# Kernel tuning notes

Measured on AMD Instinct MI355X. Metric: run time of the kernel, lower is better.

## Reference

```python
import jax, jax.numpy as jnp
import numpy as np

B, S, HID = 1, 2048, 2048
H, KV, D = 16, 8, 128          # heads, kv heads, head_dim
EPS = 1e-6
THETA_T, THETA_HW = 1000000.0, 10000.0
SCALE = D ** -0.5
NEG = -1e9


def _rms(x, w):
    xf = x.astype(jnp.float32)
    var = jnp.mean(xf * xf, axis=-1, keepdims=True)
    return (w * (xf * jax.lax.rsqrt(var + EPS))).astype(x.dtype)


def _rope_cs(pos, theta, half_dim):
    # Module builds RoPE with head_dim = 2*half_dim then takes every-other freq:
    # exponents arange(0, 2*half_dim, 4) / (2*half_dim)  -> half_dim//2 freqs
    dim2 = 2 * half_dim
    inv_freq = 1.0 / theta ** (jnp.arange(0, dim2, 4, dtype=jnp.float32) / dim2)
    freqs = pos.astype(jnp.float32)[:, None] * inv_freq[None, :]   # [S, half_dim//2]
    emb = jnp.concatenate([freqs, freqs], axis=-1)                 # [S, half_dim]
    return jnp.cos(emb), jnp.sin(emb)


def _rot_half(x):
    d = x.shape[-1] // 2
    return jnp.concatenate([-x[..., d:], x[..., :d]], axis=-1)


def _apply_rope(q, k, cos, sin):
    cos = cos[None, None]  # [1,1,S,dim]
    sin = sin[None, None]
    return q * cos + _rot_half(q) * sin, k * cos + _rot_half(k) * sin


def setup_inputs() -> dict:
    key = jax.random.key(0)
    ks = jax.random.split(key, 10)
    hidden_states = jax.random.normal(ks[0], (B, S, HID), jnp.float32)
    indexes = jax.random.randint(ks[1], (3, S), 0, S)
    causal = jnp.tril(jnp.ones((S, S), bool))
    attention_mask = jnp.where(causal, 0.0, NEG).astype(jnp.float32)[None, None]
    qkv_w = jax.random.normal(ks[2], ((H + 2 * KV) * D, HID), jnp.float32) * 0.02
    qkv_b = jax.random.normal(ks[3], ((H + 2 * KV) * D,), jnp.float32) * 0.02
    o_w = jax.random.normal(ks[4], (HID, H * D), jnp.float32) * 0.02
    o_b = jax.random.normal(ks[5], (HID,), jnp.float32) * 0.02
    q_norm_w = jnp.ones((D // 2,), jnp.float32)
    k_norm_w = jnp.ones((D // 2,), jnp.float32)
    q_norm_hw_w = jnp.ones((D // 2,), jnp.float32)
    k_norm_hw_w = jnp.ones((D // 2,), jnp.float32)
    return dict(hidden_states=hidden_states, indexes=indexes, attention_mask=attention_mask,
                qkv_w=qkv_w, qkv_b=qkv_b, o_w=o_w, o_b=o_b,
                q_norm_w=q_norm_w, k_norm_w=k_norm_w,
                q_norm_hw_w=q_norm_hw_w, k_norm_hw_w=k_norm_hw_w)


def reference(hidden_states, indexes, attention_mask, qkv_w, qkv_b, o_w, o_b,
              q_norm_w, k_norm_w, q_norm_hw_w, k_norm_hw_w):
    b, s, _ = hidden_states.shape
    qkv = hidden_states @ qkv_w.T + qkv_b
    q, k, v = jnp.split(qkv, [H * D, H * D + KV * D], axis=-1)
    q = q.reshape(b, s, H, D)
    k = k.reshape(b, s, KV, D)
    v = v.reshape(b, s, KV, D)

    # split head_dim into time half and hw half
    q_t, q_hw = jnp.split(q, 2, axis=-1)
    k_t, k_hw = jnp.split(k, 2, axis=-1)
    q_t = jnp.swapaxes(_rms(q_t, q_norm_w), 1, 2)       # [B,H,S,D/2]
    k_t = jnp.swapaxes(_rms(k_t, k_norm_w), 1, 2)
    q_hw = jnp.swapaxes(_rms(q_hw, q_norm_hw_w), 1, 2)
    k_hw = jnp.swapaxes(_rms(k_hw, k_norm_hw_w), 1, 2)
    q_h, q_ww = jnp.split(q_hw, 2, axis=-1)             # [B,H,S,D/4]
    k_h, k_ww = jnp.split(k_hw, 2, axis=-1)

    cos_t, sin_t = _rope_cs(indexes[0], THETA_T, D // 2)
    q_t, k_t = _apply_rope(q_t, k_t, cos_t, sin_t)
    cos_h, sin_h = _rope_cs(indexes[1], THETA_HW, D // 4)
    q_h, k_h = _apply_rope(q_h, k_h, cos_h, sin_h)
    cos_w, sin_w = _rope_cs(indexes[2], THETA_HW, D // 4)
    q_ww, k_ww = _apply_rope(q_ww, k_ww, cos_w, sin_w)

    query = jnp.concatenate([q_t, q_h, q_ww], axis=-1)  # [B,H,S,D]
    keyst = jnp.concatenate([k_t, k_h, k_ww], axis=-1)  # [B,KV,S,D]
    value = jnp.swapaxes(v, 1, 2)                       # [B,KV,S,D]

    n_rep = H // KV
    keyst = jnp.repeat(keyst, n_rep, axis=1)
    value = jnp.repeat(value, n_rep, axis=1)

    scores = jnp.einsum('bhsd,bhtd->bhst', query, keyst) * SCALE + attention_mask
    probs = jax.nn.softmax(scores.astype(jnp.float32), axis=-1).astype(query.dtype)
    attn = jnp.einsum('bhst,bhtd->bhsd', probs, value)
    attn = jnp.swapaxes(attn, 1, 2).reshape(b, s, H * D)
    return attn @ o_w.T + o_b
```

## Files before the change

### kernel.cpp

```cpp
#include <hip/hip_runtime.h>

typedef __bf16 bf16;
typedef __bf16 bf16x4 __attribute__((ext_vector_type(4)));
typedef __bf16 bf16x8 __attribute__((ext_vector_type(8)));
typedef float f32x4 __attribute__((ext_vector_type(4)));

#define S_LEN 2048
#define HIDDEN 2048
#define NH 16
#define NKV 8
#define HD 128
#define QKV_N 4096

__device__ __forceinline__ void async_load16(const void* g, void* l) {
  __builtin_amdgcn_global_load_lds((const __attribute__((address_space(1))) unsigned int*)g,
                                   (__attribute__((address_space(3))) unsigned int*)l,
                                   16, 0, 0);
}

template <int C>
__device__ __forceinline__ float dpp_f(float x) {
  return __builtin_bit_cast(float, __builtin_amdgcn_mov_dpp(
      __builtin_bit_cast(int, x), C, 0xF, 0xF, true));
}
__device__ __forceinline__ float rowmax16(float x) {
  x = fmaxf(x, dpp_f<0x128>(x));
  x = fmaxf(x, dpp_f<0x124>(x));
  x = fmaxf(x, dpp_f<0x122>(x));
  x = fmaxf(x, dpp_f<0x121>(x));
  return x;
}
__device__ __forceinline__ float rowsum16(float x) {
  x += dpp_f<0x128>(x);
  x += dpp_f<0x124>(x);
  x += dpp_f<0x122>(x);
  x += dpp_f<0x121>(x);
  return x;
}

__global__ __launch_bounds__(256)
void cvt2(const float* __restrict__ a, bf16* __restrict__ da, int na,
          const float* __restrict__ b, bf16* __restrict__ db) {
  int i = (blockIdx.x * 256 + threadIdx.x) * 4;
  const float* s;
  bf16* d;
  if (i < na) { s = a + i; d = da + i; }
  else        { s = b + (i - na); d = db + (i - na); }
  float4 v = *(const float4*)s;
  bf16x4 o = {(bf16)v.x, (bf16)v.y, (bf16)v.z, (bf16)v.w};
  *(bf16x4*)d = o;
}

__global__ __launch_bounds__(256)
void cvt_f32_bf16(const float* __restrict__ src, bf16* __restrict__ dst, int n) {
  int i = (blockIdx.x * 256 + threadIdx.x) * 4;
  if (i < n) {
    float4 v = *(const float4*)(src + i);
    bf16x4 o = {(bf16)v.x, (bf16)v.y, (bf16)v.z, (bf16)v.w};
    *(bf16x4*)(dst + i) = o;
  }
}

template <int WRITE_BF16>
__global__ __launch_bounds__(256)
void gemm_bt(const bf16* __restrict__ A, const bf16* __restrict__ B,
             const float* __restrict__ bias, void* __restrict__ Cout,
             int M, int N, int K) {
  __shared__ bf16 As[8192];
  __shared__ bf16 Bs[8192];
  const int tid = threadIdx.x;
  const int w = tid >> 6, lane = tid & 63;
  const int quad = lane >> 4, l15 = lane & 15;
  const int wm = w >> 1, wn = w & 1;
  const int m0 = blockIdx.y * 128, n0 = blockIdx.x * 128;

  f32x4 acc[4][4];
#pragma unroll
  for (int i = 0; i < 4; i++)
#pragma unroll
    for (int j = 0; j < 4; j++) acc[i][j] = (f32x4){0.f, 0.f, 0.f, 0.f};

  for (int k0 = 0; k0 < K; k0 += 64) {
    __syncthreads();
#pragma unroll
    for (int q = 0; q < 4; q++) {
      int i = 2 * w + (q >> 1), kc = q & 1;
      async_load16(A + (size_t)(m0 + i * 16 + l15) * K + k0 + kc * 32 + quad * 8,
                   (char*)As + (4 * w + q) * 1024);
      async_load16(B + (size_t)(n0 + i * 16 + l15) * K + k0 + kc * 32 + quad * 8,
                   (char*)Bs + (4 * w + q) * 1024);
    }
    __asm__ __volatile__("s_waitcnt vmcnt(0)" ::: "memory");
    __syncthreads();
#pragma unroll
    for (int kc = 0; kc < 2; kc++) {
      bf16x8 af[4], bfr[4];
#pragma unroll
      for (int i = 0; i < 4; i++)
        af[i] = *(const bf16x8*)((const char*)As + ((wm * 4 + i) * 2 + kc) * 1024 + lane * 16);
#pragma unroll
      for (int j = 0; j < 4; j++)
        bfr[j] = *(const bf16x8*)((const char*)Bs + ((wn * 4 + j) * 2 + kc) * 1024 + lane * 16);
#pragma unroll
      for (int i = 0; i < 4; i++)
#pragma unroll
        for (int j = 0; j < 4; j++)
          acc[i][j] = __builtin_amdgcn_mfma_f32_16x16x32_bf16(af[i], bfr[j], acc[i][j], 0, 0, 0);
    }
  }

#pragma unroll
  for (int i = 0; i < 4; i++) {
#pragma unroll
    for (int j = 0; j < 4; j++) {
      int col = n0 + wn * 64 + j * 16 + l15;
      float bv = bias[col];
#pragma unroll
      for (int r = 0; r < 4; r++) {
        int row = m0 + wm * 64 + i * 16 + quad * 4 + r;
        float v = acc[i][j][r] + bv;
        if (WRITE_BF16)
          ((bf16*)Cout)[(size_t)row * N + col] = (bf16)v;
        else
          ((float*)Cout)[(size_t)row * N + col] = v;
      }
    }
  }
}

__global__ __launch_bounds__(256)
void gemm_bt64(const bf16* __restrict__ A, const bf16* __restrict__ B,
               const float* __restrict__ bias, float* __restrict__ Cout,
               int M, int N, int K) {
  __shared__ bf16 As[8192];
  __shared__ bf16 Bs[4096];
  const int tid = threadIdx.x;
  const int w = tid >> 6, lane = tid & 63;
  const int quad = lane >> 4, l15 = lane & 15;
  const int m0 = blockIdx.y * 128, n0 = blockIdx.x * 64;

  f32x4 acc[2][4];
#pragma unroll
  for (int i = 0; i < 2; i++)
#pragma unroll
    for (int j = 0; j < 4; j++) acc[i][j] = (f32x4){0.f, 0.f, 0.f, 0.f};

  for (int k0 = 0; k0 < K; k0 += 64) {
    __syncthreads();
#pragma unroll
    for (int q = 0; q < 4; q++) {
      int i = 2 * w + (q >> 1), kc = q & 1;
      async_load16(A + (size_t)(m0 + i * 16 + l15) * K + k0 + kc * 32 + quad * 8,
                   (char*)As + (4 * w + q) * 1024);
    }
#pragma unroll
    for (int q = 0; q < 2; q++) {
      async_load16(B + (size_t)(n0 + w * 16 + l15) * K + k0 + q * 32 + quad * 8,
                   (char*)Bs + (2 * w + q) * 1024);
    }
    __asm__ __volatile__("s_waitcnt vmcnt(0)" ::: "memory");
    __syncthreads();
#pragma unroll
    for (int kc = 0; kc < 2; kc++) {
      bf16x8 af[2], bfr[4];
#pragma unroll
      for (int i = 0; i < 2; i++)
        af[i] = *(const bf16x8*)((const char*)As + ((2 * w + i) * 2 + kc) * 1024 + lane * 16);
#pragma unroll
      for (int j = 0; j < 4; j++)
        bfr[j] = *(const bf16x8*)((const char*)Bs + (j * 2 + kc) * 1024 + lane * 16);
#pragma unroll
      for (int i = 0; i < 2; i++)
#pragma unroll
        for (int j = 0; j < 4; j++)
          acc[i][j] = __builtin_amdgcn_mfma_f32_16x16x32_bf16(af[i], bfr[j], acc[i][j], 0, 0, 0);
    }
  }

#pragma unroll
  for (int i = 0; i < 2; i++) {
#pragma unroll
    for (int j = 0; j < 4; j++) {
      int col = n0 + j * 16 + l15;
      float bv = bias[col];
#pragma unroll
      for (int r = 0; r < 4; r++) {
        int row = m0 + w * 32 + i * 16 + quad * 4 + r;
        Cout[(size_t)row * N + col] = acc[i][j][r] + bv;
      }
    }
  }
}

__global__ __launch_bounds__(128)
void normrope(const bf16* __restrict__ qkv, const int* __restrict__ idx,
              const float* __restrict__ qnw, const float* __restrict__ knw,
              const float* __restrict__ qnhw, const float* __restrict__ knhw,
              bf16* __restrict__ Qb, bf16* __restrict__ Kb) {
  const int s = blockIdx.x;
  const int y = blockIdx.y;
  const int d = threadIdx.x;

  const bool isq = (y < 16);
  const int off = isq ? (y * HD + d) : (2048 + (y - 16) * HD + d);
  float x = (float)qkv[(size_t)s * QKV_N + off];

  float ss = x * x;
#pragma unroll
  for (int o = 32; o; o >>= 1) ss += __shfl_xor(ss, o);
  float inv = rsqrtf(ss * (1.f / 64.f) + 1e-6f);
  const float* wt = (d < 64) ? (isq ? qnw : knw) : (isq ? qnhw : knhw);
  float yn = x * inv * wt[d & 63];

  float pos, invf;
  int xorm;
  bool firsthalf;
  if (d < 64) {
    pos = (float)idx[s];
    int i = d & 31;
    invf = exp2f(-(float)i * 0.6228615177913804f);
    xorm = 32;
    firsthalf = (d < 32);
  } else {
    int j = d - 64;
    int region = j >> 5;
    pos = (float)idx[(1 + region) * S_LEN + s];
    int i = j & 15;
    invf = exp2f(-(float)i * 0.8304820237218406f);
    xorm = 16;
    firsthalf = ((j & 31) < 16);
  }
  float ang = pos * invf;
  float si = __sinf(ang), co = __cosf(ang);
  float partner = __shfl_xor(yn, xorm);
  float outv = firsthalf ? (yn * co - partner * si) : (yn * co + partner * si);

  if (isq)
    Qb[((size_t)y * S_LEN + s) * HD + d] = (bf16)(outv * 0.12751745f);
  else
    Kb[((size_t)(y - 16) * S_LEN + s) * HD + d] = (bf16)outv;
}

__global__ __launch_bounds__(256)
void vtrans(const bf16* __restrict__ qkv, bf16* __restrict__ VT) {
  __shared__ bf16 T[64][72];
  const int tid = threadIdx.x;
  const int s0 = blockIdx.x * 64, d0 = blockIdx.y * 64, kv = blockIdx.z;
#pragma unroll
  for (int it = 0; it < 2; it++) {
    int r = (tid >> 3) + it * 32;
    int c = (tid & 7) * 8;
    bf16x8 v = *(const bf16x8*)(qkv + (size_t)(s0 + r) * QKV_N + 3072 + kv * HD + d0 + c);
    *(bf16x8*)(&T[r][c]) = v;
  }
  __syncthreads();
#pragma unroll
  for (int it = 0; it < 2; it++) {
    int r = (tid >> 3) + it * 32;
    int c = (tid & 7) * 8;
    bf16x8 o;
#pragma unroll
    for (int j = 0; j < 8; j++) o[j] = T[c + j][r];
    *(bf16x8*)(VT + ((size_t)kv * HD + d0 + r) * S_LEN + s0 + c) = o;
  }
}

__global__ __launch_bounds__(256)
void attn_fused(const bf16* __restrict__ Qb, const bf16* __restrict__ Kb,
                const bf16* __restrict__ VT, bf16* __restrict__ attnO) {
  __shared__ bf16 Kbuf[2][8192];
  __shared__ bf16 Vbuf[8192];
  __shared__ __align__(16) bf16 Ps[4][16][72];
  const int tid = threadIdx.x;
  const int w = tid >> 6, lane = tid & 63;
  const int quad = lane >> 4, l15 = lane & 15;
  const int b = blockIdx.x;
  const int h = b & 15;
  const int g = b >> 4;
  const int qb64 = (g < 16) ? (31 - g) : (g - 16);
  const int nT = qb64 + 1;
  const int qr0 = qb64 * 64 + w * 16;
  const int kv = h >> 1;

  const bf16* Qg = Qb + (size_t)h * S_LEN * HD;
  const bf16* Kg = Kb + (size_t)kv * S_LEN * HD;
  const bf16* Vg = VT + (size_t)kv * HD * S_LEN;

  const bf16* ksrc = Kg + (size_t)(w * 16 + l15) * HD + quad * 8;
  const bf16* vsrc = Vg + (size_t)(2 * w * 16 + l15) * S_LEN + quad * 8;

  bf16x8 aq[4];
#pragma unroll
  for (int kc = 0; kc < 4; kc++)
    aq[kc] = *(const bf16x8*)(Qg + (size_t)(qr0 + l15) * HD + kc * 32 + quad * 8);

  float m2[4], li[4];
  f32x4 Oacc[8];
#pragma unroll
  for (int r = 0; r < 4; r++) { m2[r] = -1e30f; li[r] = 0.f; }
#pragma unroll
  for (int dt = 0; dt < 8; dt++) Oacc[dt] = (f32x4){0.f, 0.f, 0.f, 0.f};

#pragma unroll
  for (int kc = 0; kc < 4; kc++)
    async_load16(ksrc + kc * 32, (char*)Kbuf[0] + (w * 4 + kc) * 1024);

  for (int tt = 0; tt < nT; ++tt) {
    const int t0 = tt << 6;
    const int cur = tt & 1;
    const bool more = (tt + 1 < nT);
    __asm__ __volatile__("s_waitcnt vmcnt(0)" ::: "memory");
    __syncthreads();

#pragma unroll
    for (int e = 0; e < 2; e++)
#pragma unroll
      for (int half = 0; half < 2; half++)
        async_load16(vsrc + (size_t)e * 16 * S_LEN + t0 + half * 32,
                     (char*)Vbuf + (half * 8 + 2 * w + e) * 1024);
    if (more) {
#pragma unroll
      for (int kc = 0; kc < 4; kc++)
        async_load16(ksrc + (size_t)(t0 + 64) * HD + kc * 32,
                     (char*)Kbuf[cur ^ 1] + (w * 4 + kc) * 1024);
    }

    f32x4 sacc[4];
#pragma unroll
    for (int nt = 0; nt < 4; nt++) {
      sacc[nt] = (f32x4){0.f, 0.f, 0.f, 0.f};
#pragma unroll
      for (int kc = 0; kc < 4; kc++) {
        bf16x8 bk = *(const bf16x8*)((const char*)Kbuf[cur] + (nt * 4 + kc) * 1024 + lane * 16);
        sacc[nt] = __builtin_amdgcn_mfma_f32_16x16x32_bf16(aq[kc], bk, sacc[nt], 0, 0, 0);
      }
    }

    const bool full = (t0 + 64 <= qr0);
#pragma unroll
    for (int r = 0; r < 4; r++) {
      const int mrow = qr0 + quad * 4 + r;
      float s0 = sacc[0][r], s1 = sacc[1][r];
      float s2 = sacc[2][r], s3 = sacc[3][r];
      if (!full) {
        int cb = t0 + l15;
        if (cb > mrow) s0 = -1e30f;
        if (cb + 16 > mrow) s1 = -1e30f;
        if (cb + 32 > mrow) s2 = -1e30f;
        if (cb + 48 > mrow) s3 = -1e30f;
      }
      float mx = rowmax16(fmaxf(fmaxf(s0, s1), fmaxf(s2, s3)));
      float mnew = fmaxf(m2[r], mx);
      float alpha = exp2f(m2[r] - mnew);
      float p0 = exp2f(s0 - mnew), p1 = exp2f(s1 - mnew);
      float p2 = exp2f(s2 - mnew), p3 = exp2f(s3 - mnew);
      float rs = rowsum16((p0 + p1) + (p2 + p3));
      li[r] = li[r] * alpha + rs;
      m2[r] = mnew;
#pragma unroll
      for (int dt = 0; dt < 8; dt++) Oacc[dt][r] *= alpha;
      Ps[w][quad * 4 + r][l15] = (bf16)p0;
      Ps[w][quad * 4 + r][16 + l15] = (bf16)p1;
      Ps[w][quad * 4 + r][32 + l15] = (bf16)p2;
      Ps[w][quad * 4 + r][48 + l15] = (bf16)p3;
    }
    __asm__ __volatile__("s_waitcnt lgkmcnt(0)" ::: "memory");
    if (more)
      __asm__ __volatile__("s_waitcnt vmcnt(4)" ::: "memory");
    else
      __asm__ __volatile__("s_waitcnt vmcnt(0)" ::: "memory");

#pragma unroll
    for (int half = 0; half < 2; half++) {
      bf16x8 ap = *(const bf16x8*)(&Ps[w][l15][half * 32 + quad * 8]);
#pragma unroll
      for (int dt = 0; dt < 8; dt++) {
        bf16x8 bv = *(const bf16x8*)((const char*)Vbuf + (half * 8 + dt) * 1024 + lane * 16);
        Oacc[dt] = __builtin_amdgcn_mfma_f32_16x16x32_bf16(ap, bv, Oacc[dt], 0, 0, 0);
      }
    }
  }

#pragma unroll
  for (int r = 0; r < 4; r++) {
    float invl = 1.f / li[r];
    int srow = qr0 + quad * 4 + r;
#pragma unroll
    for (int dt = 0; dt < 8; dt++)
      attnO[(size_t)srow * HIDDEN + h * HD + dt * 16 + l15] = (bf16)(Oacc[dt][r] * invl);
  }
}

extern "C" void kernel_launch(void* const* d_in, const int* in_sizes, int n_in,
                              void* d_out, int out_size, void* d_ws, size_t ws_size,
                              hipStream_t stream) {
  const float* hidden = (const float*)d_in[0];
  const int* idx = (const int*)d_in[1];
  const float* qkv_w = (const float*)d_in[3];
  const float* qkv_b = (const float*)d_in[4];
  const float* o_w = (const float*)d_in[5];
  const float* o_b = (const float*)d_in[6];
  const float* qnw = (const float*)d_in[7];
  const float* knw = (const float*)d_in[8];
  const float* qnhw = (const float*)d_in[9];
  const float* knhw = (const float*)d_in[10];

  char* ws = (char*)d_ws;
  bf16* hB   = (bf16*)(ws);
  bf16* qwB  = (bf16*)(ws + (8u << 20));
  bf16* qkvB = (bf16*)(ws + (24u << 20));
  bf16* Qb   = (bf16*)(ws + (40u << 20));
  bf16* Kb   = (bf16*)(ws + (48u << 20));
  bf16* VT   = (bf16*)(ws + (52u << 20));
  bf16* owB  = hB;
  bf16* attn = qwB;

  const int nH = HIDDEN * S_LEN;
  const int nW = QKV_N * HIDDEN;
  cvt2<<<(nH + nW) / 1024, 256, 0, stream>>>(hidden, hB, nH, qkv_w, qwB);

  gemm_bt<1><<<dim3(QKV_N / 128, S_LEN / 128), 256, 0, stream>>>(
      hB, qwB, qkv_b, qkvB, S_LEN, QKV_N, HIDDEN);

  cvt_f32_bf16<<<HIDDEN * HIDDEN / 1024, 256, 0, stream>>>(o_w, owB, HIDDEN * HIDDEN);

  normrope<<<dim3(S_LEN, 24), 128, 0, stream>>>(qkvB, idx, qnw, knw, qnhw, knhw, Qb, Kb);
  vtrans<<<dim3(S_LEN / 64, HD / 64, NKV), 256, 0, stream>>>(qkvB, VT);

  attn_fused<<<512, 256, 0, stream>>>(Qb, Kb, VT, attn);

  gemm_bt64<<<dim3(HIDDEN / 64, S_LEN / 128), 256, 0, stream>>>(
      attn, owB, o_b, (float*)d_out, S_LEN, HIDDEN, HIDDEN);
}
```

Baseline: 321.0 us.

## Double-buffer GEMM LDS tiles and stage attention K prefetch through registers

Both GEMM kernels now keep two LDS buffers for the A and B tiles. The next K-slice is issued asynchronously before the current slice's MFMAs run, so global loads overlap with compute instead of stalling each iteration. The attention kernel goes the other way on K: it keeps a single K buffer, loads the next K tile into registers, and writes it to LDS after an extra barrier once the scores are computed. This frees LDS for occupancy but adds a synchronisation and extra register pressure, and the GEMMs now use twice the LDS, which may reduce occupancy.

```diff
diff --git a/kernel.cpp b/kernel.cpp
--- a/kernel.cpp
+++ b/kernel.cpp
@@ -66,8 +66,8 @@
 void gemm_bt(const bf16* __restrict__ A, const bf16* __restrict__ B,
              const float* __restrict__ bias, void* __restrict__ Cout,
              int M, int N, int K) {
-  __shared__ bf16 As[8192];
-  __shared__ bf16 Bs[8192];
+  __shared__ bf16 As[2][8192];
+  __shared__ bf16 Bs[2][8192];
   const int tid = threadIdx.x;
   const int w = tid >> 6, lane = tid & 63;
   const int quad = lane >> 4, l15 = lane & 15;
@@ -80,27 +80,40 @@
 #pragma unroll
     for (int j = 0; j < 4; j++) acc[i][j] = (f32x4){0.f, 0.f, 0.f, 0.f};
 
-  for (int k0 = 0; k0 < K; k0 += 64) {
-    __syncthreads();
-#pragma unroll
-    for (int q = 0; q < 4; q++) {
-      int i = 2 * w + (q >> 1), kc = q & 1;
-      async_load16(A + (size_t)(m0 + i * 16 + l15) * K + k0 + kc * 32 + quad * 8,
-                   (char*)As + (4 * w + q) * 1024);
-      async_load16(B + (size_t)(n0 + i * 16 + l15) * K + k0 + kc * 32 + quad * 8,
-                   (char*)Bs + (4 * w + q) * 1024);
-    }
+  const int nK = K >> 6;
+#pragma unroll
+  for (int q = 0; q < 4; q++) {
+    int i = 2 * w + (q >> 1), kc = q & 1;
+    async_load16(A + (size_t)(m0 + i * 16 + l15) * K + kc * 32 + quad * 8,
+                 (char*)As[0] + (4 * w + q) * 1024);
+    async_load16(B + (size_t)(n0 + i * 16 + l15) * K + kc * 32 + quad * 8,
+                 (char*)Bs[0] + (4 * w + q) * 1024);
+  }
+
+  for (int kk = 0; kk < nK; kk++) {
+    const int cur = kk & 1;
     __asm__ __volatile__("s_waitcnt vmcnt(0)" ::: "memory");
     __syncthreads();
+    if (kk + 1 < nK) {
+      const int k0n = (kk + 1) << 6;
+#pragma unroll
+      for (int q = 0; q < 4; q++) {
+        int i = 2 * w + (q >> 1), kc = q & 1;
+        async_load16(A + (size_t)(m0 + i * 16 + l15) * K + k0n + kc * 32 + quad * 8,
+                     (char*)As[cur ^ 1] + (4 * w + q) * 1024);
+        async_load16(B + (size_t)(n0 + i * 16 + l15) * K + k0n + kc * 32 + quad * 8,
+                     (char*)Bs[cur ^ 1] + (4 * w + q) * 1024);
+      }
+    }
 #pragma unroll
     for (int kc = 0; kc < 2; kc++) {
       bf16x8 af[4], bfr[4];
 #pragma unroll
       for (int i = 0; i < 4; i++)
-        af[i] = *(const bf16x8*)((const char*)As + ((wm * 4 + i) * 2 + kc) * 1024 + lane * 16);
+        af[i] = *(const bf16x8*)((const char*)As[cur] + ((wm * 4 + i) * 2 + kc) * 1024 + lane * 16);
 #pragma unroll
       for (int j = 0; j < 4; j++)
-        bfr[j] = *(const bf16x8*)((const char*)Bs + ((wn * 4 + j) * 2 + kc) * 1024 + lane * 16);
+        bfr[j] = *(const bf16x8*)((const char*)Bs[cur] + ((wn * 4 + j) * 2 + kc) * 1024 + lane * 16);
 #pragma unroll
       for (int i = 0; i < 4; i++)
 #pragma unroll
@@ -132,8 +145,8 @@
 void gemm_bt64(const bf16* __restrict__ A, const bf16* __restrict__ B,
                const float* __restrict__ bias, float* __restrict__ Cout,
                int M, int N, int K) {
-  __shared__ bf16 As[8192];
-  __shared__ bf16 Bs[4096];
+  __shared__ bf16 As[2][8192];
+  __shared__ bf16 Bs[2][4096];
   const int tid = threadIdx.x;
   const int w = tid >> 6, lane = tid & 63;
   const int quad = lane >> 4, l15 = lane & 15;
@@ -145,30 +158,44 @@
 #pragma unroll
     for (int j = 0; j < 4; j++) acc[i][j] = (f32x4){0.f, 0.f, 0.f, 0.f};
 
-  for (int k0 = 0; k0 < K; k0 += 64) {
-    __syncthreads();
-#pragma unroll
-    for (int q = 0; q < 4; q++) {
-      int i = 2 * w + (q >> 1), kc = q & 1;
-      async_load16(A + (size_t)(m0 + i * 16 + l15) * K + k0 + kc * 32 + quad * 8,
-                   (char*)As + (4 * w + q) * 1024);
-    }
-#pragma unroll
-    for (int q = 0; q < 2; q++) {
-      async_load16(B + (size_t)(n0 + w * 16 + l15) * K + k0 + q * 32 + quad * 8,
-                   (char*)Bs + (2 * w + q) * 1024);
-    }
+  const int nK = K >> 6;
+#pragma unroll
+  for (int q = 0; q < 4; q++) {
+    int i = 2 * w + (q >> 1), kc = q & 1;
+    async_load16(A + (size_t)(m0 + i * 16 + l15) * K + kc * 32 + quad * 8,
+                 (char*)As[0] + (4 * w + q) * 1024);
+  }
+#pragma unroll
+  for (int q = 0; q < 2; q++)
+    async_load16(B + (size_t)(n0 + w * 16 + l15) * K + q * 32 + quad * 8,
+                 (char*)Bs[0] + (2 * w + q) * 1024);
+
+  for (int kk = 0; kk < nK; kk++) {
+    const int cur = kk & 1;
     __asm__ __volatile__("s_waitcnt vmcnt(0)" ::: "memory");
     __syncthreads();
+    if (kk + 1 < nK) {
+      const int k0n = (kk + 1) << 6;
+#pragma unroll
+      for (int q = 0; q < 4; q++) {
+        int i = 2 * w + (q >> 1), kc = q & 1;
+        async_load16(A + (size_t)(m0 + i * 16 + l15) * K + k0n + kc * 32 + quad * 8,
+                     (char*)As[cur ^ 1] + (4 * w + q) * 1024);
+      }
+#pragma unroll
+      for (int q = 0; q < 2; q++)
+        async_load16(B + (size_t)(n0 + w * 16 + l15) * K + k0n + q * 32 + quad * 8,
+                     (char*)Bs[cur ^ 1] + (2 * w + q) * 1024);
+    }
 #pragma unroll
     for (int kc = 0; kc < 2; kc++) {
       bf16x8 af[2], bfr[4];
 #pragma unroll
       for (int i = 0; i < 2; i++)
-        af[i] = *(const bf16x8*)((const char*)As + ((2 * w + i) * 2 + kc) * 1024 + lane * 16);
+        af[i] = *(const bf16x8*)((const char*)As[cur] + ((2 * w + i) * 2 + kc) * 1024 + lane * 16);
 #pragma unroll
       for (int j = 0; j < 4; j++)
-        bfr[j] = *(const bf16x8*)((const char*)Bs + (j * 2 + kc) * 1024 + lane * 16);
+        bfr[j] = *(const bf16x8*)((const char*)Bs[cur] + (j * 2 + kc) * 1024 + lane * 16);
 #pragma unroll
       for (int i = 0; i < 2; i++)
 #pragma unroll
@@ -268,7 +295,7 @@
 __global__ __launch_bounds__(256)
 void attn_fused(const bf16* __restrict__ Qb, const bf16* __restrict__ Kb,
                 const bf16* __restrict__ VT, bf16* __restrict__ attnO) {
-  __shared__ bf16 Kbuf[2][8192];
+  __shared__ bf16 Kbuf[8192];
   __shared__ bf16 Vbuf[8192];
   __shared__ __align__(16) bf16 Ps[4][16][72];
   const int tid = threadIdx.x;
@@ -303,13 +330,12 @@
 
 #pragma unroll
   for (int kc = 0; kc < 4; kc++)
-    async_load16(ksrc + kc * 32, (char*)Kbuf[0] + (w * 4 + kc) * 1024);
+    async_load16(ksrc + kc * 32, (char*)Kbuf + (w * 4 + kc) * 1024);
+  __asm__ __volatile__("s_waitcnt vmcnt(0)" ::: "memory");
 
   for (int tt = 0; tt < nT; ++tt) {
     const int t0 = tt << 6;
-    const int cur = tt & 1;
     const bool more = (tt + 1 < nT);
-    __asm__ __volatile__("s_waitcnt vmcnt(0)" ::: "memory");
     __syncthreads();
 
 #pragma unroll
@@ -318,11 +344,12 @@
       for (int half = 0; half < 2; half++)
         async_load16(vsrc + (size_t)e * 16 * S_LEN + t0 + half * 32,
                      (char*)Vbuf + (half * 8 + 2 * w + e) * 1024);
+
+    bf16x8 knext[4];
     if (more) {
-#pragma unroll
-      for (int kc = 0; kc < 4; kc++)
-        async_load16(ksrc + (size_t)(t0 + 64) * HD + kc * 32,
-                     (char*)Kbuf[cur ^ 1] + (w * 4 + kc) * 1024);
+      const bf16* kn = ksrc + (size_t)(t0 + 64) * HD;
+#pragma unroll
+      for (int kc = 0; kc < 4; kc++) knext[kc] = *(const bf16x8*)(kn + kc * 32);
     }
 
     f32x4 sacc[4];
@@ -331,10 +358,11 @@
       sacc[nt] = (f32x4){0.f, 0.f, 0.f, 0.f};
 #pragma unroll
       for (int kc = 0; kc < 4; kc++) {
-        bf16x8 bk = *(const bf16x8*)((const char*)Kbuf[cur] + (nt * 4 + kc) * 1024 + lane * 16);
+        bf16x8 bk = *(const bf16x8*)((const char*)Kbuf + (nt * 4 + kc) * 1024 + lane * 16);
         sacc[nt] = __builtin_amdgcn_mfma_f32_16x16x32_bf16(aq[kc], bk, sacc[nt], 0, 0, 0);
       }
     }
+    __syncthreads();
 
     const bool full = (t0 + 64 <= qr0);
 #pragma unroll
@@ -365,10 +393,13 @@
       Ps[w][quad * 4 + r][48 + l15] = (bf16)p3;
     }
     __asm__ __volatile__("s_waitcnt lgkmcnt(0)" ::: "memory");
-    if (more)
-      __asm__ __volatile__("s_waitcnt vmcnt(4)" ::: "memory");
-    else
-      __asm__ __volatile__("s_waitcnt vmcnt(0)" ::: "memory");
+    __asm__ __volatile__("s_waitcnt vmcnt(0)" ::: "memory");
+
+    if (more) {
+#pragma unroll
+      for (int kc = 0; kc < 4; kc++)
+        *(bf16x8*)((char*)Kbuf + (w * 4 + kc) * 1024 + lane * 16) = knext[kc];
+    }
 
 #pragma unroll
     for (int half = 0; half < 2; half++) {
```

Result: slower. 343.1 us (+6.9%).
